# Performance work log

Measured on AMD Instinct MI355X. Metric: run time of the kernel, lower is better.

## Reference

```python
import jax, jax.numpy as jnp
import numpy as np

B, T, D, H, K = 2, 1024, 1024, 16, 64
DMIX, DDEC, DA = 32, 64, 64
EPS = 1e-5 * 64  # GroupNorm eps = 1e-5 * head_size_divisor**2


def setup_inputs() -> dict:
    keys = jax.random.split(jax.random.key(0), 12)
    r01 = 12.0 / 23.0   # layer_id / (num_hidden_layers - 1)
    r1a0 = 0.5          # 1 - layer_id / num_hidden_layers
    ddd = np.arange(D, dtype=np.float32) / D
    maa = lambda p: jnp.asarray((1.0 - ddd ** p).reshape(1, 1, D), jnp.float32)
    decay = -6.0 + 5.0 * (np.arange(D, dtype=np.float32) / (D - 1)) ** (0.7 + 1.3 * r01)
    u = lambda i, s: jax.random.uniform(keys[i], s, jnp.float32, -0.01, 0.01)
    lin = lambda i: jax.random.normal(keys[i], (D, D), jnp.float32) / np.sqrt(D)
    return dict(
        x=jax.random.normal(keys[0], (B, T, D), jnp.float32),
        time_maa_x=maa(r1a0), time_maa_w=maa(r1a0), time_maa_k=maa(r1a0),
        time_maa_v=jnp.asarray((1.0 - (ddd ** r1a0 + 0.3 * r01)).reshape(1, 1, D), jnp.float32),
        time_maa_r=maa(0.5 * r1a0), time_maa_g=maa(0.5 * r1a0), time_maa_a=maa(r1a0),
        time_maa_w1=u(1, (D, DMIX * 6)), time_maa_w2=u(2, (6, DMIX, D)),
        time_decay=jnp.asarray(decay.reshape(1, 1, D), jnp.float32),
        time_decay_w1=u(3, (D, DDEC)), time_decay_w2=u(4, (DDEC, D)),
        a0=jnp.zeros((1, 1, D), jnp.float32),
        a1=u(5, (D, DA)) * 10.0,
        a2=jax.random.normal(keys[6], (DA, D), jnp.float32) * 0.1,
        k_k=jnp.full((1, 1, D), 0.85, jnp.float32),
        k_a=jnp.ones((1, 1, D), jnp.float32),
        W_r=lin(7), W_k=lin(8), W_v=lin(9), W_g=lin(10), W_o=lin(11),
        ln_w=jnp.ones((D,), jnp.float32), ln_b=jnp.zeros((D,), jnp.float32),
    )


def reference(x, time_maa_x, time_maa_w, time_maa_k, time_maa_v, time_maa_r,
              time_maa_g, time_maa_a, time_maa_w1, time_maa_w2, time_decay,
              time_decay_w1, time_decay_w2, a0, a1, a2, k_k, k_a,
              W_r, W_k, W_v, W_g, W_o, ln_w, ln_b):
    Bx, Tx, Dx = x.shape
    # bidirectional token shift: mean of left/right neighbors
    left = jnp.pad(x[:, :-1], ((0, 0), (1, 0), (0, 0)))
    right = jnp.pad(x[:, 1:], ((0, 0), (0, 1), (0, 0)))
    dxprev = (left + right) * 0.5 - x

    # data-dependent mixing coefficients (6-way LoRA)
    xxx = x + dxprev * time_maa_x
    hmix = jnp.tanh(xxx @ time_maa_w1).reshape(Bx, Tx, 6, DMIX)
    mix = jnp.einsum('btsm,smd->sbtd', hmix, time_maa_w2)  # (6,B,T,D)
    mw, mk, mv, mr, mg, ma = mix
    xw = x + dxprev * (time_maa_w + mw)
    xk = x + dxprev * (time_maa_k + mk)
    xv = x + dxprev * (time_maa_v + mv)
    xr = x + dxprev * (time_maa_r + mr)
    xg = x + dxprev * (time_maa_g + mg)
    xa = x + dxprev * (time_maa_a + ma)

    r = xr @ W_r
    k = xk @ W_k
    v = xv @ W_v
    g = jax.nn.silu(xg @ W_g)
    w = time_decay + jnp.tanh(xw @ time_decay_w1) @ time_decay_w2
    iclr = jax.nn.sigmoid(a0 + (xa @ a1) @ a2)
    kkh = (k * k_k).reshape(Bx, Tx, H, K)
    kk = kkh / jnp.maximum(jnp.linalg.norm(kkh, axis=-1, keepdims=True), 1e-12)
    kk = kk.reshape(Bx, Tx, Dx)
    k = k * (1.0 + (iclr - 1.0) * k_a)

    heads = lambda t: t.reshape(Bx, Tx, H, K).transpose(0, 2, 1, 3)  # (B,H,T,K)
    r_h, k_h, v_h, kk_h, iclr_h = map(heads, (r, k, v, kk, iclr))
    w_h = -jnp.exp(heads(w))

    # LION bidirectional attention with delta correction (quadratic form)
    cs = jnp.cumsum(w_h, axis=2)
    cs_b = cs - w_h
    cs_f = jnp.clip(cs - cs[:, :, Tx // 2:Tx // 2 + 1, :], -60.0, 60.0)
    cs_bs = jnp.clip(cs_b - cs_b[:, :, Tx // 2:Tx // 2 + 1, :], -60.0, 60.0)
    A_fwd = jnp.tril(jnp.einsum('bhik,bhjk->bhij', r_h * jnp.exp(cs_f), k_h * jnp.exp(-cs_f)))
    A_bwd = jnp.triu(jnp.einsum('bhik,bhjk->bhij', r_h * jnp.exp(-cs_bs), k_h * jnp.exp(cs_bs)), k=1)
    kk_corr = jnp.einsum('bhik,bhjk->bhij', kk_h * iclr_h, kk_h)
    A_df = -jnp.tril(A_fwd @ jnp.tril(kk_corr, -1))
    A_db = -jnp.triu(A_bwd @ jnp.triu(kk_corr, 1), k=1)
    y = (A_fwd + A_bwd + A_df + A_db) @ v_h  # (B,H,T,K)

    # GroupNorm(n_head groups) over flattened tokens
    y = y.transpose(0, 2, 1, 3).reshape(Bx * Tx, H, K)
    mu = y.mean(axis=-1, keepdims=True)
    var = y.var(axis=-1, keepdims=True)
    y = (y - mu) / jnp.sqrt(var + EPS)
    y = y.reshape(Bx, Tx, Dx) * ln_w + ln_b
    return (y * g) @ W_o
```

## Files before the change

kernel.cpp:

```cpp
#include <hip/hip_runtime.h>
#include <math.h>

#define BB 2
#define TT 1024
#define DD 1024
#define HH 16
#define KK 64
#define NBT 2048
#define NE  2097152ULL

typedef unsigned short u16;
typedef __attribute__((ext_vector_type(8))) short short8;
typedef __attribute__((ext_vector_type(4))) short short4v;
typedef __attribute__((ext_vector_type(4))) float f32x4;

__device__ __forceinline__ float bf2f(u16 u) {
  union { unsigned int i; float f; } v; v.i = ((unsigned int)u) << 16; return v.f;
}
__device__ __forceinline__ u16 f2bf(float x) {
  union { float f; unsigned int u; } v; v.f = x;
  unsigned int r = v.u + 0x7fffu + ((v.u >> 16) & 1u);
  return (u16)(r >> 16);
}
__device__ __forceinline__ f32x4 MFMA(short8 a, short8 b, f32x4 c) {
  return __builtin_amdgcn_mfma_f32_16x16x32_bf16(a, b, c, 0, 0, 0);
}
__device__ __forceinline__ int swzb(int row, int kbyte) {
  return row * 128 + (kbyte ^ ((row & 7) << 4));
}
__device__ __forceinline__ void gload16(const void* g, void* l) {
  __builtin_amdgcn_global_load_lds((const __attribute__((address_space(1))) void*)g,
                                   (__attribute__((address_space(3))) void*)l, 16, 0, 0);
}

__global__ __launch_bounds__(256)
void pre(const float* __restrict__ W2, u16* __restrict__ W2t,
         const float* __restrict__ W1, u16* __restrict__ W1t,
         const float* __restrict__ wdec2, const float* __restrict__ a2,
         u16* __restrict__ wdec2t, u16* __restrict__ a2t,
         const float* __restrict__ wdec1, const float* __restrict__ a1,
         u16* __restrict__ wdec1t, u16* __restrict__ a1t,
         const float* __restrict__ x, const float* __restrict__ maa_x,
         u16* __restrict__ xxx_b) {
  __shared__ float tl[64][65];
  int idx = blockIdx.x;
  int tid = threadIdx.x;
  if (idx < 96) {
    int s = idx >> 4, d0 = (idx & 15) * 64;
    int c = tid & 63, r0 = (tid >> 6) * 8;
#pragma unroll
    for (int j = 0; j < 8; ++j)
      tl[r0 + j][c] = W2[(size_t)(s * 32 + r0 + j) * 1024 + d0 + c];
    __syncthreads();
    int d = tid >> 2, ms = (tid & 3) * 8;
    u16 o[8];
#pragma unroll
    for (int j = 0; j < 8; ++j) o[j] = f2bf(tl[ms + j][d]);
    *(short8*)(W2t + ((size_t)s * 1024 + d0 + d) * 32 + ms) = *(short8*)o;
  } else if (idx < 144) {
    int i = idx - 96;
    int k0 = (i & 15) * 64, n0 = (i >> 4) * 64;
    int r = tid >> 2, c0 = (tid & 3) * 16;
#pragma unroll
    for (int j = 0; j < 16; j += 4) {
      f32x4 v = *(const f32x4*)(W1 + (size_t)(k0 + r) * 192 + n0 + c0 + j);
      tl[r][c0 + j + 0] = v[0]; tl[r][c0 + j + 1] = v[1];
      tl[r][c0 + j + 2] = v[2]; tl[r][c0 + j + 3] = v[3];
    }
    __syncthreads();
    u16 o[16];
#pragma unroll
    for (int j = 0; j < 16; ++j) o[j] = f2bf(tl[c0 + j][r]);
    *(short8*)(W1t + (size_t)(n0 + r) * 1024 + k0 + c0) = *(short8*)(o);
    *(short8*)(W1t + (size_t)(n0 + r) * 1024 + k0 + c0 + 8) = *(short8*)(o + 8);
  } else if (idx < 176) {
    int i = idx - 144;
    int zz = i >> 4;
    const float* W = zz ? a2 : wdec2;
    u16* Wt = zz ? a2t : wdec2t;
    int n0 = (i & 15) * 64;
    int r = tid >> 2, c0 = (tid & 3) * 16;
#pragma unroll
    for (int j = 0; j < 16; j += 4) {
      f32x4 v = *(const f32x4*)(W + (size_t)r * 1024 + n0 + c0 + j);
      tl[r][c0 + j + 0] = v[0]; tl[r][c0 + j + 1] = v[1];
      tl[r][c0 + j + 2] = v[2]; tl[r][c0 + j + 3] = v[3];
    }
    __syncthreads();
    u16 o[16];
#pragma unroll
    for (int j = 0; j < 16; ++j) o[j] = f2bf(tl[c0 + j][r]);
    *(short8*)(Wt + (size_t)(n0 + r) * 64 + c0) = *(short8*)(o);
    *(short8*)(Wt + (size_t)(n0 + r) * 64 + c0 + 8) = *(short8*)(o + 8);
  } else if (idx < 208) {
    int i = idx - 176;
    int zz = i >> 4;
    const float* W = zz ? a1 : wdec1;
    u16* Wt = zz ? a1t : wdec1t;
    int k0 = (i & 15) * 64;
    int r = tid >> 2, c0 = (tid & 3) * 16;
#pragma unroll
    for (int j = 0; j < 16; j += 4) {
      f32x4 v = *(const f32x4*)(W + (size_t)(k0 + r) * 64 + c0 + j);
      tl[r][c0 + j + 0] = v[0]; tl[r][c0 + j + 1] = v[1];
      tl[r][c0 + j + 2] = v[2]; tl[r][c0 + j + 3] = v[3];
    }
    __syncthreads();
    u16 o[16];
#pragma unroll
    for (int j = 0; j < 16; ++j) o[j] = f2bf(tl[c0 + j][r]);
    *(short8*)(Wt + (size_t)r * 1024 + k0 + c0) = *(short8*)(o);
    *(short8*)(Wt + (size_t)r * 1024 + k0 + c0 + 8) = *(short8*)(o + 8);
  } else {
    int row = idx - 208;
    int t = row & (TT - 1);
    int d0 = tid * 4;
    size_t g = (size_t)row * DD + d0;
    f32x4 xc = *(const f32x4*)(x + g);
    f32x4 xl = {0.f, 0.f, 0.f, 0.f}, xr = {0.f, 0.f, 0.f, 0.f};
    if (t != 0) xl = *(const f32x4*)(x + g - DD);
    if (t != TT - 1) xr = *(const f32x4*)(x + g + DD);
    f32x4 mx = *(const f32x4*)(maa_x + d0);
    u16 o[4];
#pragma unroll
    for (int j = 0; j < 4; ++j)
      o[j] = f2bf(xc[j] + (0.5f * (xl[j] + xr[j]) - xc[j]) * mx[j]);
    *(short4v*)(xxx_b + g) = *(short4v*)o;
  }
}

__global__ __launch_bounds__(256)
void hmix_g(const float* __restrict__ W_r, const float* __restrict__ W_k,
            const float* __restrict__ W_v, const float* __restrict__ W_g,
            const float* __restrict__ W_o,
            u16* __restrict__ TR, u16* __restrict__ TK, u16* __restrict__ TV,
            u16* __restrict__ TG, u16* __restrict__ TO,
            const u16* __restrict__ xxx_b, const u16* __restrict__ W1t,
            float* __restrict__ P3) {
  __shared__ float tl[64][65];
  __shared__ u16 As[4096];
  __shared__ u16 Bs[2048];
  int idx = blockIdx.x;
  int tid = threadIdx.x;
  if (idx < 1280) {
    int z = idx >> 8, rem = idx & 255;
    const float* W = (z == 0) ? W_r : (z == 1) ? W_k : (z == 2) ? W_v : (z == 3) ? W_g : W_o;
    u16* Wt = (z == 0) ? TR : (z == 1) ? TK : (z == 2) ? TV : (z == 3) ? TG : TO;
    int k0 = (rem & 15) * 64, n0 = (rem >> 4) * 64;
    int r = tid >> 2, c0 = (tid & 3) * 16;
#pragma unroll
    for (int j = 0; j < 16; j += 4) {
      f32x4 v = *(const f32x4*)(W + (size_t)(k0 + r) * 1024 + n0 + c0 + j);
      tl[r][c0 + j + 0] = v[0]; tl[r][c0 + j + 1] = v[1];
      tl[r][c0 + j + 2] = v[2]; tl[r][c0 + j + 3] = v[3];
    }
    __syncthreads();
    u16 o[16];
#pragma unroll
    for (int j = 0; j < 16; ++j) o[j] = f2bf(tl[c0 + j][r]);
    *(short8*)(Wt + (size_t)(n0 + r) * 1024 + k0 + c0) = *(short8*)(o);
    *(short8*)(Wt + (size_t)(n0 + r) * 1024 + k0 + c0 + 8) = *(short8*)(o + 8);
    return;
  }
  int i = idx - 1280;
  int n0 = (i % 3) * 64;
  int q = i / 3;
  int m0 = (q & 15) * 128;
  int kb = q >> 4;
  int w = tid >> 6, lane = tid & 63;
  int mq = w >> 1, nq = w & 1;
  f32x4 acc[4][2];
#pragma unroll
  for (int ii = 0; ii < 4; ++ii)
#pragma unroll
    for (int j = 0; j < 2; ++j) acc[ii][j] = {0.f, 0.f, 0.f, 0.f};
  for (int t = 0; t < 4; ++t) {
    int k0 = kb * 128 + t * 32;
#pragma unroll
    for (int c2 = 0; c2 < 2; ++c2) {
      int ch = w * 2 + c2;
      int row = ch * 16 + (lane >> 2);
      gload16(xxx_b + (size_t)(m0 + row) * 1024 + k0 + (lane & 3) * 8, As + ch * 512);
    }
    {
      int row = w * 16 + (lane >> 2);
      gload16(W1t + (size_t)(n0 + row) * 1024 + k0 + (lane & 3) * 8, Bs + w * 512);
    }
    __syncthreads();
    short8 a[4], b[2];
#pragma unroll
    for (int mf = 0; mf < 4; ++mf)
      a[mf] = *(const short8*)(As + (mq * 64 + mf * 16 + (lane & 15)) * 32 + (lane >> 4) * 8);
#pragma unroll
    for (int nf = 0; nf < 2; ++nf)
      b[nf] = *(const short8*)(Bs + (nq * 32 + nf * 16 + (lane & 15)) * 32 + (lane >> 4) * 8);
#pragma unroll
    for (int mf = 0; mf < 4; ++mf)
#pragma unroll
      for (int nf = 0; nf < 2; ++nf) acc[mf][nf] = MFMA(a[mf], b[nf], acc[mf][nf]);
    __syncthreads();
  }
#pragma unroll
  for (int mf = 0; mf < 4; ++mf) {
#pragma unroll
    for (int nf = 0; nf < 2; ++nf) {
      int mb = m0 + mq * 64 + mf * 16 + (lane >> 4) * 4;
      int n = n0 + nq * 32 + nf * 16 + (lane & 15);
#pragma unroll
      for (int r = 0; r < 4; ++r)
        P3[(size_t)kb * 393216 + (size_t)(mb + r) * 192 + n] = acc[mf][nf][r];
    }
  }
}

__global__ __launch_bounds__(256)
void reduce8b(const float* __restrict__ P, u16* __restrict__ C, int total) {
  size_t i = (size_t)blockIdx.x * 256 + threadIdx.x;
  float s = 0.f;
#pragma unroll
  for (int kb = 0; kb < 8; ++kb) s += P[(size_t)kb * total + i];
  C[i] = f2bf(tanhf(s));
}

__global__ __launch_bounds__(256)
void reduce8_pairb(const float* __restrict__ Pw, const float* __restrict__ Pa,
                   u16* __restrict__ hdec_b, u16* __restrict__ ha_b) {
  int z = blockIdx.y;
  size_t i = (size_t)blockIdx.x * 256 + threadIdx.x;
  const float* P = z ? Pa : Pw;
  float s = 0.f;
#pragma unroll
  for (int kb = 0; kb < 8; ++kb) s += P[(size_t)kb * 131072 + i];
  if (z) ha_b[i] = f2bf(s);
  else hdec_b[i] = f2bf(tanhf(s));
}

__global__ __launch_bounds__(256)
void mixg(const u16* __restrict__ hmixb, const u16* __restrict__ W2t,
          const float* __restrict__ x,
          const float* __restrict__ maa_w, const float* __restrict__ maa_k,
          const float* __restrict__ maa_v, const float* __restrict__ maa_r,
          const float* __restrict__ maa_g, const float* __restrict__ maa_a,
          u16* __restrict__ xw_b, u16* __restrict__ xa_b,
          u16* __restrict__ xk_b, u16* __restrict__ xv_b,
          u16* __restrict__ xr_b, u16* __restrict__ xg_b) {
  __shared__ u16 shm[16384];
  u16* As = shm;
  u16* Bs = shm + 4096;
  u16* mixt = shm;
  int s = blockIdx.z;
  int m0 = blockIdx.y * 128, n0 = blockIdx.x * 128;
  int tid = threadIdx.x, w = tid >> 6, lane = tid & 63;
  int mq = w >> 1, nq = w & 1;
#pragma unroll
  for (int c2 = 0; c2 < 2; ++c2) {
    int ch = w * 2 + c2;
    int row = ch * 16 + (lane >> 2);
    gload16(hmixb + (size_t)(m0 + row) * 192 + s * 32 + (lane & 3) * 8, As + ch * 512);
    gload16(W2t + ((size_t)s * 1024 + n0 + row) * 32 + (lane & 3) * 8, Bs + ch * 512);
  }
  __syncthreads();
  short8 a[4], b[4];
#pragma unroll
  for (int mf = 0; mf < 4; ++mf)
    a[mf] = *(const short8*)(As + (mq * 64 + mf * 16 + (lane & 15)) * 32 + (lane >> 4) * 8);
#pragma unroll
  for (int nf = 0; nf < 4; ++nf)
    b[nf] = *(const short8*)(Bs + (nq * 64 + nf * 16 + (lane & 15)) * 32 + (lane >> 4) * 8);
  f32x4 acc[4][4];
#pragma unroll
  for (int mf = 0; mf < 4; ++mf)
#pragma unroll
    for (int nf = 0; nf < 4; ++nf) {
      f32x4 z = {0.f, 0.f, 0.f, 0.f};
      acc[mf][nf] = MFMA(a[mf], b[nf], z);
    }
  __syncthreads();
#pragma unroll
  for (int mf = 0; mf < 4; ++mf) {
#pragma unroll
    for (int nf = 0; nf < 4; ++nf) {
      int col = nq * 64 + nf * 16 + (lane & 15);
#pragma unroll
      for (int r = 0; r < 4; ++r) {
        int row = mq * 64 + mf * 16 + (lane >> 4) * 4 + r;
        mixt[row * 128 + col] = f2bf(acc[mf][nf][r]);
      }
    }
  }
  __syncthreads();
  const float* maa = (s == 0) ? maa_w : (s == 1) ? maa_k : (s == 2) ? maa_v
                    : (s == 3) ? maa_r : (s == 4) ? maa_g : maa_a;
  u16* dst = (s == 0) ? xw_b : (s == 1) ? xk_b : (s == 2) ? xv_b
            : (s == 3) ? xr_b : (s == 4) ? xg_b : xa_b;
  int cg = tid & 15;
  int rowg = tid >> 4;
  int d0 = n0 + cg * 8;
  f32x4 ma0 = *(const f32x4*)(maa + d0);
  f32x4 ma1 = *(const f32x4*)(maa + d0 + 4);
#pragma unroll
  for (int rr = 0; rr < 8; ++rr) {
    int row = rr * 16 + rowg;
    int m = m0 + row;
    int t = m & (TT - 1);
    size_t g = (size_t)m * DD + d0;
    f32x4 xc0 = *(const f32x4*)(x + g);
    f32x4 xc1 = *(const f32x4*)(x + g + 4);
    f32x4 xl0 = {0.f, 0.f, 0.f, 0.f}, xl1 = {0.f, 0.f, 0.f, 0.f};
    f32x4 xr0 = {0.f, 0.f, 0.f, 0.f}, xr1 = {0.f, 0.f, 0.f, 0.f};
    if (t != 0) { xl0 = *(const f32x4*)(x + g - DD); xl1 = *(const f32x4*)(x + g - DD + 4); }
    if (t != TT - 1) { xr0 = *(const f32x4*)(x + g + DD); xr1 = *(const f32x4*)(x + g + DD + 4); }
    short8 mv = *(const short8*)(mixt + row * 128 + cg * 8);
    u16 o[8];
#pragma unroll
    for (int j = 0; j < 8; ++j) {
      float xcj = (j < 4) ? xc0[j & 3] : xc1[j & 3];
      float xlj = (j < 4) ? xl0[j & 3] : xl1[j & 3];
      float xrj = (j < 4) ? xr0[j & 3] : xr1[j & 3];
      float maj = (j < 4) ? ma0[j & 3] : ma1[j & 3];
      float dx = 0.5f * (xlj + xrj) - xcj;
      o[j] = f2bf(xcj + dx * (maj + bf2f((u16)mv[j])));
    }
    *(short8*)(dst + g) = *(short8*)o;
  }
}

__global__ __launch_bounds__(256)
void gemm_bf4(const u16* __restrict__ xr, const u16* __restrict__ xk,
              const u16* __restrict__ xv, const u16* __restrict__ xg,
              const u16* __restrict__ WtR, const u16* __restrict__ WtK,
              const u16* __restrict__ WtV, const u16* __restrict__ WtG,
              u16* __restrict__ rbuf, u16* __restrict__ kbuf,
              u16* __restrict__ vT, u16* __restrict__ gb,
              const u16* __restrict__ xw_b, const u16* __restrict__ wdec1t,
              float* __restrict__ PpartW,
              const u16* __restrict__ xa_b, const u16* __restrict__ a1t,
              float* __restrict__ PpartA) {
  __shared__ u16 As[2][4096];
  __shared__ u16 Bs[2][2048];
  int wgid = blockIdx.x;
  int tid = threadIdx.x, w = tid >> 6, lane = tid & 63;
  int mq = w >> 1, nq = w & 1;
  if (wgid >= 1024) {
    int i = wgid - 1024;
    int m0 = (i & 15) * 128;
    int kb = (i >> 4) & 7;
    int z = i >> 7;
    const u16* A = z ? xa_b : xw_b;
    const u16* Bt = z ? a1t : wdec1t;
    float* P = z ? PpartA : PpartW;
    f32x4 acc[4][2];
#pragma unroll
    for (int ii = 0; ii < 4; ++ii)
#pragma unroll
      for (int j = 0; j < 2; ++j) acc[ii][j] = {0.f, 0.f, 0.f, 0.f};
    for (int t = 0; t < 4; ++t) {
      int k0 = kb * 128 + t * 32;
#pragma unroll
      for (int c2 = 0; c2 < 2; ++c2) {
        int ch = w * 2 + c2;
        int row = ch * 16 + (lane >> 2);
        gload16(A + (size_t)(m0 + row) * 1024 + k0 + (lane & 3) * 8, As[0] + ch * 512);
      }
      {
        int row = w * 16 + (lane >> 2);
        gload16(Bt + (size_t)row * 1024 + k0 + (lane & 3) * 8, Bs[0] + w * 512);
      }
      __syncthreads();
      short8 a[4], b[2];
#pragma unroll
      for (int mf = 0; mf < 4; ++mf)
        a[mf] = *(const short8*)(As[0] + (mq * 64 + mf * 16 + (lane & 15)) * 32 + (lane >> 4) * 8);
#pragma unroll
      for (int nf = 0; nf < 2; ++nf)
        b[nf] = *(const short8*)(Bs[0] + (nq * 32 + nf * 16 + (lane & 15)) * 32 + (lane >> 4) * 8);
#pragma unroll
      for (int mf = 0; mf < 4; ++mf)
#pragma unroll
        for (int nf = 0; nf < 2; ++nf) acc[mf][nf] = MFMA(a[mf], b[nf], acc[mf][nf]);
      __syncthreads();
    }
#pragma unroll
    for (int mf = 0; mf < 4; ++mf) {
#pragma unroll
      for (int nf = 0; nf < 2; ++nf) {
        int mb = m0 + mq * 64 + mf * 16 + (lane >> 4) * 4;
        int n = nq * 32 + nf * 16 + (lane & 15);
#pragma unroll
        for (int r = 0; r < 4; ++r)
          P[(size_t)kb * 131072 + (size_t)(mb + r) * 64 + n] = acc[mf][nf][r];
      }
    }
    return;
  }
  int xcd = wgid & 7, idx = wgid >> 3;
  int z = xcd >> 1, mhalf = xcd & 1;
  int mloc = idx & 7, nt = idx >> 3;
  int m0 = (mhalf * 8 + mloc) * 128;
  int n0 = nt * 64;
  const u16* A = (z == 0) ? xr : (z == 1) ? xk : (z == 2) ? xv : xg;
  const u16* Bt = (z == 0) ? WtR : (z == 1) ? WtK : (z == 2) ? WtV : WtG;
  int arow0 = (w * 2) * 16 + (lane >> 2);
  int arow1 = (w * 2 + 1) * 16 + (lane >> 2);
  int brow = w * 16 + (lane >> 2);
  int kc = (lane & 3) * 8;
  f32x4 acc[4][2];
#pragma unroll
  for (int i = 0; i < 4; ++i)
#pragma unroll
    for (int j = 0; j < 2; ++j) acc[i][j] = {0.f, 0.f, 0.f, 0.f};
  gload16(A + (size_t)(m0 + arow0) * 1024 + kc, As[0] + (w * 2) * 512);
  gload16(A + (size_t)(m0 + arow1) * 1024 + kc, As[0] + (w * 2 + 1) * 512);
  gload16(Bt + (size_t)(n0 + brow) * 1024 + kc, Bs[0] + w * 512);
  __syncthreads();
  for (int t = 0; t < 32; ++t) {
    int cur = t & 1;
    if (t < 31) {
      int kn = (t + 1) * 32;
      gload16(A + (size_t)(m0 + arow0) * 1024 + kn + kc, As[cur ^ 1] + (w * 2) * 512);
      gload16(A + (size_t)(m0 + arow1) * 1024 + kn + kc, As[cur ^ 1] + (w * 2 + 1) * 512);
      gload16(Bt + (size_t)(n0 + brow) * 1024 + kn + kc, Bs[cur ^ 1] + w * 512);
    }
    short8 a[4], b[2];
#pragma unroll
    for (int mf = 0; mf < 4; ++mf)
      a[mf] = *(const short8*)(As[cur] + (mq * 64 + mf * 16 + (lane & 15)) * 32 + (lane >> 4) * 8);
#pragma unroll
    for (int nf = 0; nf < 2; ++nf)
      b[nf] = *(const short8*)(Bs[cur] + (nq * 32 + nf * 16 + (lane & 15)) * 32 + (lane >> 4) * 8);
#pragma unroll
    for (int mf = 0; mf < 4; ++mf)
#pragma unroll
      for (int nf = 0; nf < 2; ++nf) acc[mf][nf] = MFMA(a[mf], b[nf], acc[mf][nf]);
    __syncthreads();
  }
#pragma unroll
  for (int mf = 0; mf < 4; ++mf) {
#pragma unroll
    for (int nf = 0; nf < 2; ++nf) {
      int mb = m0 + mq * 64 + mf * 16 + (lane >> 4) * 4;
      int n = n0 + nq * 32 + nf * 16 + (lane & 15);
      if (z == 2) {
        u16 o[4];
#pragma unroll
        for (int r = 0; r < 4; ++r) o[r] = f2bf(acc[mf][nf][r]);
        int b2 = mb >> 10, t = mb & 1023;
        *(short4v*)(vT + (((size_t)(b2 * HH + (n >> 6))) * KK + (n & 63)) * TT + t) = *(short4v*)o;
      } else if (z == 3) {
#pragma unroll
        for (int r = 0; r < 4; ++r) {
          int m = mb + r;
          float v = acc[mf][nf][r];
          gb[(size_t)m * 1024 + n] = f2bf(v / (1.f + __expf(-v)));
        }
      } else {
        u16* C = (z == 0) ? rbuf : kbuf;
#pragma unroll
        for (int r = 0; r < 4; ++r) {
          int m = mb + r;
          int b2 = m >> 10, t = m & 1023;
          C[(((size_t)(b2 * HH + (n >> 6))) * TT + t) * KK + (n & 63)] = f2bf(acc[mf][nf][r]);
        }
      }
    }
  }
}

__global__ __launch_bounds__(256)
void gemm_bfo(const u16* __restrict__ A, const u16* __restrict__ Bt,
              float* __restrict__ C) {
  __shared__ u16 As[2][4096];
  __shared__ u16 Bs[2][2048];
  int wgid = blockIdx.x;
  int xcd = wgid & 7, idx = wgid >> 3;
  int mloc = idx & 1, nt = idx >> 1;
  int m0 = (xcd * 2 + mloc) * 128;
  int n0 = nt * 64;
  int tid = threadIdx.x, w = tid >> 6, lane = tid & 63;
  int mq = w >> 1, nq = w & 1;
  int arow0 = (w * 2) * 16 + (lane >> 2);
  int arow1 = (w * 2 + 1) * 16 + (lane >> 2);
  int brow = w * 16 + (lane >> 2);
  int kc = (lane & 3) * 8;
  f32x4 acc[4][2];
#pragma unroll
  for (int i = 0; i < 4; ++i)
#pragma unroll
    for (int j = 0; j < 2; ++j) acc[i][j] = {0.f, 0.f, 0.f, 0.f};
  gload16(A + (size_t)(m0 + arow0) * 1024 + kc, As[0] + (w * 2) * 512);
  gload16(A + (size_t)(m0 + arow1) * 1024 + kc, As[0] + (w * 2 + 1) * 512);
  gload16(Bt + (size_t)(n0 + brow) * 1024 + kc, Bs[0] + w * 512);
  __syncthreads();
  for (int t = 0; t < 32; ++t) {
    int cur = t & 1;
    if (t < 31) {
      int kn = (t + 1) * 32;
      gload16(A + (size_t)(m0 + arow0) * 1024 + kn + kc, As[cur ^ 1] + (w * 2) * 512);
      gload16(A + (size_t)(m0 + arow1) * 1024 + kn + kc, As[cur ^ 1] + (w * 2 + 1) * 512);
      gload16(Bt + (size_t)(n0 + brow) * 1024 + kn + kc, Bs[cur ^ 1] + w * 512);
    }
    short8 a[4], b[2];
#pragma unroll
    for (int mf = 0; mf < 4; ++mf)
      a[mf] = *(const short8*)(As[cur] + (mq * 64 + mf * 16 + (lane & 15)) * 32 + (lane >> 4) * 8);
#pragma unroll
    for (int nf = 0; nf < 2; ++nf)
      b[nf] = *(const short8*)(Bs[cur] + (nq * 32 + nf * 16 + (lane & 15)) * 32 + (lane >> 4) * 8);
#pragma unroll
    for (int mf = 0; mf < 4; ++mf)
#pragma unroll
      for (int nf = 0; nf < 2; ++nf) acc[mf][nf] = MFMA(a[mf], b[nf], acc[mf][nf]);
    __syncthreads();
  }
#pragma unroll
  for (int mf = 0; mf < 4; ++mf) {
#pragma unroll
    for (int nf = 0; nf < 2; ++nf) {
      int mb = m0 + mq * 64 + mf * 16 + (lane >> 4) * 4;
      int n = n0 + nq * 32 + nf * 16 + (lane & 15);
#pragma unroll
      for (int r = 0; r < 4; ++r)
        C[(size_t)(mb + r) * 1024 + n] = acc[mf][nf][r];
    }
  }
}

__global__ __launch_bounds__(256)
void gemm_k2b(const u16* __restrict__ A0, const u16* __restrict__ B0t,
              float* __restrict__ C0, const float* __restrict__ bias0,
              const u16* __restrict__ A1, const u16* __restrict__ B1t,
              float* __restrict__ C1, const float* __restrict__ bias1) {
  __shared__ u16 As[8192];
  __shared__ u16 Bs[4096];
  int z = blockIdx.z;
  const u16* A = z ? A1 : A0;
  const u16* Bt = z ? B1t : B0t;
  float* C = z ? C1 : C0;
  const float* bias = z ? bias1 : bias0;
  int n0 = blockIdx.x * 64, m0 = blockIdx.y * 128;
  int tid = threadIdx.x, w = tid >> 6, lane = tid & 63;
  int mq = w >> 1, nq = w & 1;
#pragma unroll
  for (int j = 0; j < 4; ++j) {
    int q = w * 4 + j;
    int ks = q >> 3, rg = q & 7;
    int row = rg * 16 + (lane >> 2);
    int kc = ks * 32 + (lane & 3) * 8;
    gload16(A + (size_t)(m0 + row) * 64 + kc, As + q * 512);
  }
#pragma unroll
  for (int j = 0; j < 2; ++j) {
    int q = w * 2 + j;
    int ks = q >> 2, rg = q & 3;
    int row = rg * 16 + (lane >> 2);
    int kc = ks * 32 + (lane & 3) * 8;
    gload16(Bt + (size_t)(n0 + row) * 64 + kc, Bs + q * 512);
  }
  __syncthreads();
  f32x4 acc[4][2];
#pragma unroll
  for (int i = 0; i < 4; ++i)
#pragma unroll
    for (int j = 0; j < 2; ++j) acc[i][j] = {0.f, 0.f, 0.f, 0.f};
#pragma unroll
  for (int ks = 0; ks < 2; ++ks) {
    short8 a[4], b[2];
#pragma unroll
    for (int mf = 0; mf < 4; ++mf)
      a[mf] = *(const short8*)(As + ks * 4096 + (mq * 64 + mf * 16 + (lane & 15)) * 32 + (lane >> 4) * 8);
#pragma unroll
    for (int nf = 0; nf < 2; ++nf)
      b[nf] = *(const short8*)(Bs + ks * 2048 + (nq * 32 + nf * 16 + (lane & 15)) * 32 + (lane >> 4) * 8);
#pragma unroll
    for (int mf = 0; mf < 4; ++mf)
#pragma unroll
      for (int nf = 0; nf < 2; ++nf) acc[mf][nf] = MFMA(a[mf], b[nf], acc[mf][nf]);
  }
#pragma unroll
  for (int mf = 0; mf < 4; ++mf) {
#pragma unroll
    for (int nf = 0; nf < 2; ++nf) {
      int mb = m0 + mq * 64 + mf * 16 + (lane >> 4) * 4;
      int n = n0 + nq * 32 + nf * 16 + (lane & 15);
      float bv = bias[n];
#pragma unroll
      for (int r = 0; r < 4; ++r) {
        int m = mb + r;
        int b2 = m >> 10, t = m & 1023;
        float vv = acc[mf][nf][r] + bv;
        if (z) vv = 1.f / (1.f + expf(-vv));
        C[(((size_t)(b2 * HH + (n >> 6))) * TT + t) * KK + (n & 63)] = vv;
      }
    }
  }
}

__global__ __launch_bounds__(256)
void k4k5(u16* __restrict__ kbuf, u16* __restrict__ kkbuf, u16* __restrict__ kkibuf,
          const float* __restrict__ iclr, const float* __restrict__ k_k,
          const float* __restrict__ k_a,
          const float* __restrict__ csf, float* __restrict__ csbs,
          float* __restrict__ part) {
  int idx = blockIdx.x;
  int tid = threadIdx.x;
  if (idx < 8192) {
    int gid = idx * 4 + (tid >> 6);
    int lane = tid & 63;
    size_t base = (size_t)gid * 64 + lane;
    int h = (gid >> 10) & (HH - 1);
    int d = h * 64 + lane;
    float kv = bf2f(kbuf[base]);
    float ic = iclr[base];
    float kkh = kv * k_k[d];
    float ss = kkh * kkh;
#pragma unroll
    for (int off = 32; off > 0; off >>= 1) ss += __shfl_xor(ss, off);
    float nrm = fmaxf(sqrtf(ss), 1e-12f);
    float kkv = kkh / nrm;
    kkbuf[base] = f2bf(kkv);
    kkibuf[base] = f2bf(kkv * ic);
    kbuf[base] = f2bf(kv * (1.f + (ic - 1.f) * k_a[d]));
  } else {
    int bc = (idx - 8192) * 4 + (tid >> 6);
    int bh = bc >> 4, c = bc & 15;
    int lane = tid & 63;
    size_t base = (size_t)bh * TT * KK + (size_t)c * 64 * KK + lane;
    float p = 0.f;
    for (int i = 0; i < 64; ++i) {
      float wh = -expf(csf[base + (size_t)i * KK]);
      csbs[base + (size_t)i * KK] = wh;
      p += wh;
    }
    part[((size_t)bh * 16 + c) * 64 + lane] = p;
  }
}

struct SReg { short8 a0, a1, b0, b1; };
template <int RSA, int RSB>
__device__ __forceinline__ void sload(const u16* ka, const u16* vb, SReg& r) {
  int t0 = threadIdx.x, t1 = threadIdx.x + 256;
  r.a0 = *(const short8*)(ka + (size_t)(t0 >> 3) * RSA + (t0 & 7) * 8);
  r.a1 = *(const short8*)(ka + (size_t)(t1 >> 3) * RSA + (t1 & 7) * 8);
  r.b0 = *(const short8*)(vb + (size_t)(t0 >> 3) * RSB + (t0 & 7) * 8);
  r.b1 = *(const short8*)(vb + (size_t)(t1 >> 3) * RSB + (t1 & 7) * 8);
}
__device__ __forceinline__ void swrite(u16* Kt, u16* Vt, const SReg& r) {
  int t0 = threadIdx.x, t1 = threadIdx.x + 256;
  *(short8*)((char*)Kt + swzb(t0 >> 3, (t0 & 7) * 16)) = r.a0;
  *(short8*)((char*)Kt + swzb(t1 >> 3, (t1 & 7) * 16)) = r.a1;
  *(short8*)((char*)Vt + swzb(t0 >> 3, (t0 & 7) * 16)) = r.b0;
  *(short8*)((char*)Vt + swzb(t1 >> 3, (t1 & 7) * 16)) = r.b1;
}
template <int MASK>
__device__ __forceinline__ void store_S(const f32x4 s[4], u16* St, int lane, int w) {
  int ig0 = w * 16 + (lane >> 4) * 4;
#pragma unroll
  for (int jf = 0; jf < 4; ++jf) {
    int jl = jf * 16 + (lane & 15);
#pragma unroll
    for (int r = 0; r < 4; ++r) {
      int il = ig0 + r;
      float v = s[jf][r];
      if (MASK == 1 && !(jl < il)) v = 0.f;
      if (MASK == 2 && !(jl > il)) v = 0.f;
      if (MASK == 3 && !(jl <= il)) v = 0.f;
      *(u16*)((char*)St + swzb(il, jl * 2)) = f2bf(v);
    }
  }
}
__device__ __forceinline__ void smm(short8 a0, short8 a1, const u16* Kt, f32x4 s[4], int lane) {
  __builtin_amdgcn_s_setprio(1);
#pragma unroll
  for (int jf = 0; jf < 4; ++jf) {
    f32x4 z = {0.f, 0.f, 0.f, 0.f};
    short8 kb0 = *(const short8*)((const char*)Kt + swzb(jf * 16 + (lane & 15), (lane >> 4) * 16));
    z = MFMA(a0, kb0, z);
    short8 kb1 = *(const short8*)((const char*)Kt + swzb(jf * 16 + (lane & 15), 64 + (lane >> 4) * 16));
    z = MFMA(a1, kb1, z);
    s[jf] = z;
  }
  __builtin_amdgcn_s_setprio(0);
}
__device__ __forceinline__ void pv(const u16* St, const u16* Vt, f32x4 acc[4], int lane, int w) {
  __builtin_amdgcn_s_setprio(1);
#pragma unroll
  for (int ks = 0; ks < 2; ++ks) {
    short8 a = *(const short8*)((const char*)St + swzb(w * 16 + (lane & 15), ks * 64 + (lane >> 4) * 16));
#pragma unroll
    for (int cf = 0; cf < 4; ++cf) {
      short8 b = *(const short8*)((const char*)Vt + swzb(cf * 16 + (lane & 15), ks * 64 + (lane >> 4) * 16));
      acc[cf] = MFMA(a, b, acc[cf]);
    }
  }
  __builtin_amdgcn_s_setprio(0);
}

__global__ __launch_bounds__(256)
void k6_pass1(const u16* __restrict__ kk, const u16* __restrict__ kki,
              const u16* __restrict__ vT, u16* __restrict__ vfT, u16* __restrict__ vbT,
              const float* __restrict__ csbs, const float* __restrict__ part,
              const u16* __restrict__ rb, const u16* __restrict__ kb,
              u16* __restrict__ rfb, u16* __restrict__ rbb,
              u16* __restrict__ kfb, u16* __restrict__ kbw) {
  __shared__ u16 Kt[2][4096], Vt[2][4096], St[4096];
  int wg = blockIdx.x;
  int tid = threadIdx.x;
  if (wg >= 512) {
    int bc = (wg - 512) * 4 + (tid >> 6);
    int bh = bc >> 4, c = bc & 15;
    int lane = tid & 63;
    size_t hb = (size_t)bh * TT * KK;
    float run = 0.f, csb512 = 0.f;
    for (int cc = 0; cc < 16; ++cc) {
      float pvv = part[((size_t)bh * 16 + cc) * 64 + lane];
      if (cc < c) run += pvv;
      if (cc < 8) csb512 += pvv;
    }
    float wh512 = csbs[hb + (size_t)512 * KK + lane];
    float cs512 = csb512 + wh512;
    size_t base = hb + (size_t)c * 64 * KK + lane;
    float cs = run;
    for (int i = 0; i < 64; ++i) {
      size_t g = base + (size_t)i * KK;
      float wh = csbs[g];
      cs += wh;
      float cf = fminf(fmaxf(cs - cs512, -60.f), 60.f);
      float cb = fminf(fmaxf((cs - wh) - csb512, -60.f), 60.f);
      float rvf = bf2f(rb[g]);
      float kvf = bf2f(kb[g]);
      rfb[g] = f2bf(rvf * __expf(cf));
      kfb[g] = f2bf(kvf * __expf(-cf));
      rbb[g] = f2bf(rvf * __expf(-cb));
      kbw[g] = f2bf(kvf * __expf(cb));
    }
    return;
  }
  int bh = wg & 31, it = wg >> 5, i0 = it * 64;
  size_t hb = (size_t)bh * 65536;
  int w = tid >> 6, lane = tid & 63;
  int iw = i0 + w * 16;
  int row = iw + (lane & 15), ko = (lane >> 4) * 8;
  short8 a0 = *(const short8*)(kki + hb + (size_t)row * 64 + ko);
  short8 a1 = *(const short8*)(kki + hb + (size_t)row * 64 + 32 + ko);
  f32x4 af[4], ab[4];
#pragma unroll
  for (int c = 0; c < 4; ++c) { af[c] = {0.f, 0.f, 0.f, 0.f}; ab[c] = {0.f, 0.f, 0.f, 0.f}; }
  SReg sr, nx;
  sload<64, 1024>(kk + hb, vT + hb, sr);
  swrite(Kt[0], Vt[0], sr);
  __syncthreads();
  for (int s = 0; s < 16; ++s) {
    int cur = s & 1;
    if (s < 15)
      sload<64, 1024>(kk + hb + (size_t)(s + 1) * 4096, vT + hb + (s + 1) * 64, nx);
    f32x4 sv[4];
    smm(a0, a1, Kt[cur], sv, lane);
    if (s == it) {
      store_S<1>(sv, St, lane, w);
      pv(St, Vt[cur], af, lane, w);
      store_S<2>(sv, St, lane, w);
      pv(St, Vt[cur], ab, lane, w);
    } else if (s < it) {
      store_S<0>(sv, St, lane, w);
      pv(St, Vt[cur], af, lane, w);
    } else {
      store_S<0>(sv, St, lane, w);
      pv(St, Vt[cur], ab, lane, w);
    }
    if (s < 15) swrite(Kt[cur ^ 1], Vt[cur ^ 1], nx);
    __syncthreads();
  }
#pragma unroll
  for (int cf = 0; cf < 4; ++cf) {
    int c = cf * 16 + (lane & 15);
    int i = iw + (lane >> 4) * 4;
    size_t g = hb + (size_t)c * 1024 + i;
    short4v vv = *(const short4v*)(vT + g);
    u16 o1[4], o2[4];
#pragma unroll
    for (int r = 0; r < 4; ++r) {
      float v0 = bf2f((u16)vv[r]);
      o1[r] = f2bf(v0 - af[cf][r]);
      o2[r] = f2bf(v0 - ab[cf][r]);
    }
    *(short4v*)(vfT + g) = *(short4v*)o1;
    *(short4v*)(vbT + g) = *(short4v*)o2;
  }
}

__global__ __launch_bounds__(256)
void k7_pass2(const u16* __restrict__ rfb, const u16* __restrict__ rbb,
              const u16* __restrict__ kfb, const u16* __restrict__ kbw,
              const u16* __restrict__ vfT, const u16* __restrict__ vbT,
              float* __restrict__ y) {
  __shared__ u16 Kt[2][4096], Vt[2][4096], St[4096];
  int wg = blockIdx.x;
  int bh = wg & 31, it = wg >> 5, i0 = it * 64;
  size_t hb = (size_t)bh * 65536;
  int tid = threadIdx.x, w = tid >> 6, lane = tid & 63;
  int iw = i0 + w * 16;
  int row = iw + (lane & 15), ko = (lane >> 4) * 8;
  short8 rf0 = *(const short8*)(rfb + hb + (size_t)row * 64 + ko);
  short8 rf1 = *(const short8*)(rfb + hb + (size_t)row * 64 + 32 + ko);
  short8 rb0 = *(const short8*)(rbb + hb + (size_t)row * 64 + ko);
  short8 rb1 = *(const short8*)(rbb + hb + (size_t)row * 64 + 32 + ko);
  f32x4 acc[4];
#pragma unroll
  for (int c = 0; c < 4; ++c) acc[c] = {0.f, 0.f, 0.f, 0.f};
  SReg sr, nx;
  {
    sload<64, 1024>(kfb + hb, vfT + hb, sr);
    swrite(Kt[0], Vt[0], sr);
  }
  __syncthreads();
  for (int s = 0; s < 17; ++s) {
    int cur = s & 1;
    if (s < 16) {
      int s1 = s + 1;
      bool f1 = (s1 <= it);
      int j1 = f1 ? s1 : s1 - 1;
      const u16* kp = (f1 ? kfb : kbw) + hb + (size_t)j1 * 4096;
      const u16* vp = (f1 ? vfT : vbT) + hb + j1 * 64;
      sload<64, 1024>(kp, vp, nx);
    }
    bool fwd = (s <= it);
    int jt = fwd ? s : s - 1;
    short8 a0 = fwd ? rf0 : rb0;
    short8 a1 = fwd ? rf1 : rb1;
    f32x4 sv[4];
    smm(a0, a1, Kt[cur], sv, lane);
    if (jt == it) {
      if (fwd) store_S<3>(sv, St, lane, w);
      else store_S<2>(sv, St, lane, w);
    } else {
      store_S<0>(sv, St, lane, w);
    }
    pv(St, Vt[cur], acc, lane, w);
    if (s < 16) swrite(Kt[cur ^ 1], Vt[cur ^ 1], nx);
    __syncthreads();
  }
#pragma unroll
  for (int cf = 0; cf < 4; ++cf) {
    int c = cf * 16 + (lane & 15);
#pragma unroll
    for (int r = 0; r < 4; ++r) {
      int i = iw + (lane >> 4) * 4 + r;
      y[hb + (size_t)i * 64 + c] = acc[cf][r];
    }
  }
}

__global__ __launch_bounds__(256)
void k8_gnorm(const float* __restrict__ y, const u16* __restrict__ g,
              const float* __restrict__ lnw, const float* __restrict__ lnb,
              u16* __restrict__ outb) {
  int bt = blockIdx.x;
  int b = bt >> 10, t = bt & 1023;
  int wv = threadIdx.x >> 6, lane = threadIdx.x & 63;
  for (int h = wv; h < HH; h += 4) {
    size_t idx = (((size_t)(b * HH + h)) * TT + t) * KK + lane;
    float v = y[idx];
    float s1 = v, s2 = v * v;
#pragma unroll
    for (int off = 32; off > 0; off >>= 1) {
      s1 += __shfl_xor(s1, off);
      s2 += __shfl_xor(s2, off);
    }
    float mu = s1 * (1.f / 64.f);
    float var = s2 * (1.f / 64.f) - mu * mu;
    float xn = (v - mu) * rsqrtf(var + 6.4e-4f);
    int d = h * 64 + lane;
    float o = xn * lnw[d] + lnb[d];
    outb[(size_t)bt * DD + d] = f2bf(o * bf2f(g[(size_t)bt * DD + d]));
  }
}

extern "C" void kernel_launch(void* const* d_in, const int* in_sizes, int n_in,
                              void* d_out, int out_size, void* d_ws, size_t ws_size,
                              hipStream_t stream) {
  const float* x      = (const float*)d_in[0];
  const float* maa_x  = (const float*)d_in[1];
  const float* maa_w  = (const float*)d_in[2];
  const float* maa_k  = (const float*)d_in[3];
  const float* maa_v  = (const float*)d_in[4];
  const float* maa_r  = (const float*)d_in[5];
  const float* maa_g  = (const float*)d_in[6];
  const float* maa_a  = (const float*)d_in[7];
  const float* w1mix  = (const float*)d_in[8];
  const float* w2mix  = (const float*)d_in[9];
  const float* tdecay = (const float*)d_in[10];
  const float* wdec1  = (const float*)d_in[11];
  const float* wdec2  = (const float*)d_in[12];
  const float* a0     = (const float*)d_in[13];
  const float* a1     = (const float*)d_in[14];
  const float* a2     = (const float*)d_in[15];
  const float* k_k    = (const float*)d_in[16];
  const float* k_a    = (const float*)d_in[17];
  const float* W_r    = (const float*)d_in[18];
  const float* W_k    = (const float*)d_in[19];
  const float* W_v    = (const float*)d_in[20];
  const float* W_g    = (const float*)d_in[21];
  const float* W_o    = (const float*)d_in[22];
  const float* lnw    = (const float*)d_in[23];
  const float* lnb    = (const float*)d_in[24];
  float* out = (float*)d_out;

  const size_t NEf = NE;
  float* F = (float*)d_ws;
  u16*   xxx_b  = (u16*)F;
  float* ybuf   = F;
  u16*   xw_b   = (u16*)(F + 1 * NEf);
  u16*   xa_b   = (u16*)(F + 2 * NEf);
  float* csfb   = F + 3 * NEf;
  float* csbsb  = F + 4 * NEf;
  float* P3     = F + 3 * NEf;
  float* PpartW = F + 3 * NEf;
  float* PpartA = F + 4 * NEf;
  float* iclr   = F + 5 * NEf;
  u16*   gb     = (u16*)(F + 6 * NEf);
  u16*   hmixb  = (u16*)(F + 7 * NEf);
  u16*   hdec_b = (u16*)(F + 7 * NEf + 524288);
  u16*   ha_b   = (u16*)(F + 7 * NEf + 786432);
  float* partb  = F + 7 * NEf + 917504;
  u16*   W1t    = (u16*)(F + 7 * NEf + 1048576);
  u16*   wdec2t = (u16*)(F + 7 * NEf + 1146880);
  u16*   a2t    = (u16*)(F + 7 * NEf + 1179648);
  u16*   wdec1t = (u16*)(F + 7 * NEf + 1212416);
  u16*   a1t    = (u16*)(F + 7 * NEf + 1245184);
  u16*   W2t    = (u16*)(F + 7 * NEf + 1966080);
  u16* rfb = (u16*)xw_b;
  u16* rbb = rfb + NEf;
  u16* kfb = (u16*)xa_b;
  u16* kbw = kfb + NEf;
  u16* U = (u16*)(F + 8 * NEf);
  u16* xr_b = U + 0 * NEf;
  u16* xk_b = U + 1 * NEf;
  u16* xv_b = U + 2 * NEf;
  u16* xg_b = U + 3 * NEf;
  u16* rbuf = U + 4 * NEf;
  u16* kbuf = U + 5 * NEf;
  u16* vT   = U + 6 * NEf;
  u16* kkb  = U + 7 * NEf;
  u16* kkib = U + 8 * NEf;
  u16* vfT  = U + 9 * NEf;
  u16* vbT  = U + 10 * NEf;
  u16* gnb  = U + 11 * NEf;
  u16* WtR  = U + 12 * NEf;
  u16* WtK  = U + 12 * NEf + 1048576;
  u16* WtV  = U + 12 * NEf + 2097152;
  u16* WtG  = U + 12 * NEf + 3145728;
  u16* WtO  = U + 12 * NEf + 4194304;

  dim3 blk(256);

  pre<<<2256, blk, 0, stream>>>(w2mix, W2t, w1mix, W1t, wdec2, a2, wdec2t, a2t,
                                wdec1, a1, wdec1t, a1t, x, maa_x, xxx_b);

  hmix_g<<<1664, blk, 0, stream>>>(W_r, W_k, W_v, W_g, W_o,
                                   WtR, WtK, WtV, WtG, WtO,
                                   xxx_b, W1t, P3);
  reduce8b<<<1536, blk, 0, stream>>>(P3, hmixb, 393216);

  mixg<<<dim3(8, 16, 6), blk, 0, stream>>>(hmixb, W2t, x,
                                           maa_w, maa_k, maa_v, maa_r, maa_g, maa_a,
                                           xw_b, xa_b, xk_b, xv_b, xr_b, xg_b);

  gemm_bf4<<<1280, blk, 0, stream>>>(xr_b, xk_b, xv_b, xg_b,
                                     WtR, WtK, WtV, WtG,
                                     rbuf, kbuf, vT, gb,
                                     xw_b, wdec1t, PpartW, xa_b, a1t, PpartA);

  reduce8_pairb<<<dim3(512, 2), blk, 0, stream>>>(PpartW, PpartA, hdec_b, ha_b);
  gemm_k2b<<<dim3(16, 16, 2), blk, 0, stream>>>(hdec_b, wdec2t, csfb, tdecay,
                                                ha_b, a2t, iclr, a0);

  k4k5<<<8320, blk, 0, stream>>>(kbuf, kkb, kkib, iclr, k_k, k_a,
                                 csfb, csbsb, partb);

  k6_pass1<<<640, blk, 0, stream>>>(kkb, kkib, vT, vfT, vbT,
                                    csbsb, partb, rbuf, kbuf,
                                    rfb, rbb, kfb, kbw);
  k7_pass2<<<512, blk, 0, stream>>>(rfb, rbb, kfb, kbw, vfT, vbT, ybuf);
  k8_gnorm<<<NBT, blk, 0, stream>>>(ybuf, gb, lnw, lnb, gnb);
  gemm_bfo<<<256, blk, 0, stream>>>(gnb, WtO, out);
}
```

Before: 184.6 us.

## Split attention passes into separate forward/backward workgroups and skip masked tiles

k6_pass1 and k7_pass2 now launch separate workgroups for the forward (causal) and backward (anti-causal) directions. Each workgroup iterates only over the key tiles on its side of the diagonal instead of all 16 or 17. The two direction outputs go to separate y buffers, and the GroupNorm kernel sums them when it loads. This doubles the number of workgroups to fill more CUs and removes fully masked tile work, but the workgroups become imbalanced and the extra y buffer adds memory traffic.

After: 178.6 us. 1.03x faster.

```diff
diff --git a/kernel.cpp b/kernel.cpp
--- a/kernel.cpp
+++ b/kernel.cpp
@@ -705,8 +705,8 @@
   __shared__ u16 Kt[2][4096], Vt[2][4096], St[4096];
   int wg = blockIdx.x;
   int tid = threadIdx.x;
-  if (wg >= 512) {
-    int bc = (wg - 512) * 4 + (tid >> 6);
+  if (wg >= 1024) {
+    int bc = (wg - 1024) * 4 + (tid >> 6);
     int bh = bc >> 4, c = bc & 15;
     int lane = tid & 63;
     size_t hb = (size_t)bh * TT * KK;
@@ -735,56 +735,53 @@
     }
     return;
   }
-  int bh = wg & 31, it = wg >> 5, i0 = it * 64;
+  int dir = (wg >= 512);
+  int w0 = dir ? wg - 512 : wg;
+  int bh = w0 & 31, it = w0 >> 5, i0 = it * 64;
   size_t hb = (size_t)bh * 65536;
   int w = tid >> 6, lane = tid & 63;
   int iw = i0 + w * 16;
   int row = iw + (lane & 15), ko = (lane >> 4) * 8;
   short8 a0 = *(const short8*)(kki + hb + (size_t)row * 64 + ko);
   short8 a1 = *(const short8*)(kki + hb + (size_t)row * 64 + 32 + ko);
-  f32x4 af[4], ab[4];
-#pragma unroll
-  for (int c = 0; c < 4; ++c) { af[c] = {0.f, 0.f, 0.f, 0.f}; ab[c] = {0.f, 0.f, 0.f, 0.f}; }
+  f32x4 acc[4];
+#pragma unroll
+  for (int c = 0; c < 4; ++c) acc[c] = {0.f, 0.f, 0.f, 0.f};
+  int s0 = dir ? it : 0;
+  int nph = dir ? 16 - it : it + 1;
   SReg sr, nx;
-  sload<64, 1024>(kk + hb, vT + hb, sr);
+  sload<64, 1024>(kk + hb + (size_t)s0 * 4096, vT + hb + s0 * 64, sr);
   swrite(Kt[0], Vt[0], sr);
   __syncthreads();
-  for (int s = 0; s < 16; ++s) {
-    int cur = s & 1;
-    if (s < 15)
+  for (int p = 0; p < nph; ++p) {
+    int s = s0 + p;
+    int cur = p & 1;
+    if (p < nph - 1)
       sload<64, 1024>(kk + hb + (size_t)(s + 1) * 4096, vT + hb + (s + 1) * 64, nx);
     f32x4 sv[4];
     smm(a0, a1, Kt[cur], sv, lane);
     if (s == it) {
-      store_S<1>(sv, St, lane, w);
-      pv(St, Vt[cur], af, lane, w);
-      store_S<2>(sv, St, lane, w);
-      pv(St, Vt[cur], ab, lane, w);
-    } else if (s < it) {
-      store_S<0>(sv, St, lane, w);
-      pv(St, Vt[cur], af, lane, w);
+      if (dir) store_S<2>(sv, St, lane, w);
+      else store_S<1>(sv, St, lane, w);
     } else {
       store_S<0>(sv, St, lane, w);
-      pv(St, Vt[cur], ab, lane, w);
-    }
-    if (s < 15) swrite(Kt[cur ^ 1], Vt[cur ^ 1], nx);
-    __syncthreads();
-  }
+    }
+    pv(St, Vt[cur], acc, lane, w);
+    if (p < nph - 1) swrite(Kt[cur ^ 1], Vt[cur ^ 1], nx);
+    __syncthreads();
+  }
+  u16* dst = dir ? vbT : vfT;
 #pragma unroll
   for (int cf = 0; cf < 4; ++cf) {
     int c = cf * 16 + (lane & 15);
     int i = iw + (lane >> 4) * 4;
     size_t g = hb + (size_t)c * 1024 + i;
     short4v vv = *(const short4v*)(vT + g);
-    u16 o1[4], o2[4];
-#pragma unroll
-    for (int r = 0; r < 4; ++r) {
-      float v0 = bf2f((u16)vv[r]);
-      o1[r] = f2bf(v0 - af[cf][r]);
-      o2[r] = f2bf(v0 - ab[cf][r]);
-    }
-    *(short4v*)(vfT + g) = *(short4v*)o1;
-    *(short4v*)(vbT + g) = *(short4v*)o2;
+    u16 o1[4];
+#pragma unroll
+    for (int r = 0; r < 4; ++r)
+      o1[r] = f2bf(bf2f((u16)vv[r]) - acc[cf][r]);
+    *(short4v*)(dst + g) = *(short4v*)o1;
   }
 }
 
@@ -792,53 +789,48 @@
 void k7_pass2(const u16* __restrict__ rfb, const u16* __restrict__ rbb,
               const u16* __restrict__ kfb, const u16* __restrict__ kbw,
               const u16* __restrict__ vfT, const u16* __restrict__ vbT,
-              float* __restrict__ y) {
+              float* __restrict__ yf, float* __restrict__ yb) {
   __shared__ u16 Kt[2][4096], Vt[2][4096], St[4096];
   int wg = blockIdx.x;
-  int bh = wg & 31, it = wg >> 5, i0 = it * 64;
+  int dir = (wg >= 512);
+  int w0 = dir ? wg - 512 : wg;
+  int bh = w0 & 31, it = w0 >> 5, i0 = it * 64;
   size_t hb = (size_t)bh * 65536;
   int tid = threadIdx.x, w = tid >> 6, lane = tid & 63;
   int iw = i0 + w * 16;
   int row = iw + (lane & 15), ko = (lane >> 4) * 8;
-  short8 rf0 = *(const short8*)(rfb + hb + (size_t)row * 64 + ko);
-  short8 rf1 = *(const short8*)(rfb + hb + (size_t)row * 64 + 32 + ko);
-  short8 rb0 = *(const short8*)(rbb + hb + (size_t)row * 64 + ko);
-  short8 rb1 = *(const short8*)(rbb + hb + (size_t)row * 64 + 32 + ko);
+  const u16* rp = dir ? rbb : rfb;
+  const u16* kp = dir ? kbw : kfb;
+  const u16* vp = dir ? vbT : vfT;
+  short8 a0 = *(const short8*)(rp + hb + (size_t)row * 64 + ko);
+  short8 a1 = *(const short8*)(rp + hb + (size_t)row * 64 + 32 + ko);
   f32x4 acc[4];
 #pragma unroll
   for (int c = 0; c < 4; ++c) acc[c] = {0.f, 0.f, 0.f, 0.f};
+  int s0 = dir ? it : 0;
+  int nph = dir ? 16 - it : it + 1;
   SReg sr, nx;
-  {
-    sload<64, 1024>(kfb + hb, vfT + hb, sr);
-    swrite(Kt[0], Vt[0], sr);
-  }
+  sload<64, 1024>(kp + hb + (size_t)s0 * 4096, vp + hb + s0 * 64, sr);
+  swrite(Kt[0], Vt[0], sr);
   __syncthreads();
-  for (int s = 0; s < 17; ++s) {
-    int cur = s & 1;
-    if (s < 16) {
-      int s1 = s + 1;
-      bool f1 = (s1 <= it);
-      int j1 = f1 ? s1 : s1 - 1;
-      const u16* kp = (f1 ? kfb : kbw) + hb + (size_t)j1 * 4096;
-      const u16* vp = (f1 ? vfT : vbT) + hb + j1 * 64;
-      sload<64, 1024>(kp, vp, nx);
-    }
-    bool fwd = (s <= it);
-    int jt = fwd ? s : s - 1;
-    short8 a0 = fwd ? rf0 : rb0;
-    short8 a1 = fwd ? rf1 : rb1;
+  for (int p = 0; p < nph; ++p) {
+    int s = s0 + p;
+    int cur = p & 1;
+    if (p < nph - 1)
+      sload<64, 1024>(kp + hb + (size_t)(s + 1) * 4096, vp + hb + (s + 1) * 64, nx);
     f32x4 sv[4];
     smm(a0, a1, Kt[cur], sv, lane);
-    if (jt == it) {
-      if (fwd) store_S<3>(sv, St, lane, w);
-      else store_S<2>(sv, St, lane, w);
+    if (s == it) {
+      if (dir) store_S<2>(sv, St, lane, w);
+      else store_S<3>(sv, St, lane, w);
     } else {
       store_S<0>(sv, St, lane, w);
     }
     pv(St, Vt[cur], acc, lane, w);
-    if (s < 16) swrite(Kt[cur ^ 1], Vt[cur ^ 1], nx);
-    __syncthreads();
-  }
+    if (p < nph - 1) swrite(Kt[cur ^ 1], Vt[cur ^ 1], nx);
+    __syncthreads();
+  }
+  float* y = dir ? yb : yf;
 #pragma unroll
   for (int cf = 0; cf < 4; ++cf) {
     int c = cf * 16 + (lane & 15);
@@ -851,15 +843,15 @@
 }
 
 __global__ __launch_bounds__(256)
-void k8_gnorm(const float* __restrict__ y, const u16* __restrict__ g,
-              const float* __restrict__ lnw, const float* __restrict__ lnb,
-              u16* __restrict__ outb) {
+void k8_gn2(const float* __restrict__ yf, const float* __restrict__ yb,
+            const u16* __restrict__ g, const float* __restrict__ lnw,
+            const float* __restrict__ lnb, u16* __restrict__ outb) {
   int bt = blockIdx.x;
   int b = bt >> 10, t = bt & 1023;
   int wv = threadIdx.x >> 6, lane = threadIdx.x & 63;
   for (int h = wv; h < HH; h += 4) {
     size_t idx = (((size_t)(b * HH + h)) * TT + t) * KK + lane;
-    float v = y[idx];
+    float v = yf[idx] + yb[idx];
     float s1 = v, s2 = v * v;
 #pragma unroll
     for (int off = 32; off > 0; off >>= 1) {
@@ -908,7 +900,6 @@
   const size_t NEf = NE;
   float* F = (float*)d_ws;
   u16*   xxx_b  = (u16*)F;
-  float* ybuf   = F;
   u16*   xw_b   = (u16*)(F + 1 * NEf);
   u16*   xa_b   = (u16*)(F + 2 * NEf);
   float* csfb   = F + 3 * NEf;
@@ -916,6 +907,8 @@
   float* P3     = F + 3 * NEf;
   float* PpartW = F + 3 * NEf;
   float* PpartA = F + 4 * NEf;
+  float* yf     = F + 3 * NEf;
+  float* yb     = F + 4 * NEf;
   float* iclr   = F + 5 * NEf;
   u16*   gb     = (u16*)(F + 6 * NEf);
   u16*   hmixb  = (u16*)(F + 7 * NEf);
@@ -977,10 +970,10 @@
   k4k5<<<8320, blk, 0, stream>>>(kbuf, kkb, kkib, iclr, k_k, k_a,
                                  csfb, csbsb, partb);
 
-  k6_pass1<<<640, blk, 0, stream>>>(kkb, kkib, vT, vfT, vbT,
-                                    csbsb, partb, rbuf, kbuf,
-                                    rfb, rbb, kfb, kbw);
-  k7_pass2<<<512, blk, 0, stream>>>(rfb, rbb, kfb, kbw, vfT, vbT, ybuf);
-  k8_gnorm<<<NBT, blk, 0, stream>>>(ybuf, gb, lnw, lnb, gnb);
+  k6_pass1<<<1152, blk, 0, stream>>>(kkb, kkib, vT, vfT, vbT,
+                                     csbsb, partb, rbuf, kbuf,
+                                     rfb, rbb, kfb, kbw);
+  k7_pass2<<<1024, blk, 0, stream>>>(rfb, rbb, kfb, kbw, vfT, vbT, yf, yb);
+  k8_gn2<<<NBT, blk, 0, stream>>>(yf, yb, gb, lnw, lnb, gnb);
   gemm_bfo<<<256, blk, 0, stream>>>(gnb, WtO, out);
 }
```
